# Kernel optimization log

Measured on AMD Instinct MI355X. Metric: run time of the kernel, lower is better.

The kernel has to match this reference:

```python
import jax, jax.numpy as jnp
import numpy as np

N = 100000      # nodes
E = 1600000     # graph edges
P = 800000      # hypergraph incidence pairs
HE = 20000      # hyperedges
F_IN = 128      # node features
DIM = 64        # hidden dim (hard-coded in module)
NC = 40         # num_classes


def _lin_init(key, fan_in, fan_out):
    k1, k2 = jax.random.split(key)
    s = 1.0 / np.sqrt(fan_in)
    W = jax.random.uniform(k1, (fan_in, fan_out), jnp.float32, -s, s)
    b = jax.random.uniform(k2, (fan_out,), jnp.float32, -s, s)
    return W, b


def setup_inputs() -> dict:
    key = jax.random.key(0)
    ks = jax.random.split(key, 10)
    x = jax.random.normal(ks[0], (N, F_IN), jnp.float32)
    edge_index = jax.random.randint(ks[1], (2, E), 0, N, dtype=jnp.int64)
    node_idx = jax.random.randint(ks[2], (P,), 0, N, dtype=jnp.int64)
    he_idx = jax.random.randint(ks[3], (P,), 0, HE, dtype=jnp.int64)
    hyperedge_index = jnp.stack([node_idx, he_idx], axis=0)
    W_h1, b_h1 = _lin_init(ks[4], F_IN, DIM)
    W_h2, b_h2 = _lin_init(ks[5], DIM, DIM)
    W_c1, b_c1 = _lin_init(ks[6], F_IN + DIM, DIM)
    W_c2, b_c2 = _lin_init(ks[7], DIM, NC)
    W_lp, b_lp = _lin_init(ks[8], NC, NC)
    return dict(x=x, edge_index=edge_index, hyperedge_index=hyperedge_index,
                W_h1=W_h1, b_h1=b_h1, W_h2=W_h2, b_h2=b_h2,
                W_c1=W_c1, b_c1=b_c1, W_c2=W_c2, b_c2=b_c2,
                W_lp=W_lp, b_lp=b_lp)


def hypergraph_conv(x, node_idx, he_idx, W, b):
    # PyG HypergraphConv (no attention, hyperedge_weight = 1):
    # out = D^{-1} H B^{-1} H^T (x W) + b
    xw = x @ W                                    # [N, D]
    ones = jnp.ones(node_idx.shape[0], xw.dtype)
    Dn = jax.ops.segment_sum(ones, node_idx, num_segments=N)   # node degree
    Bh = jax.ops.segment_sum(ones, he_idx, num_segments=HE)    # hyperedge size
    D_inv = jnp.where(Dn > 0, 1.0 / Dn, 0.0)
    B_inv = jnp.where(Bh > 0, 1.0 / Bh, 0.0)
    # node -> hyperedge: m_e = (1/|e|) sum_{i in e} xw[i]
    msg1 = xw[node_idx] * B_inv[he_idx][:, None]               # [P, D]
    e_feat = jax.ops.segment_sum(msg1, he_idx, num_segments=HE)
    # hyperedge -> node: out_i = (1/deg(i)) sum_{e ni i} m_e
    msg2 = e_feat[he_idx] * D_inv[node_idx][:, None]           # [P, D]
    out = jax.ops.segment_sum(msg2, node_idx, num_segments=N)
    return out + b


def gcn_conv(x, edge_index, W, b):
    # PyG GCNConv: add self-loops, symmetric normalization
    xw = x @ W                                    # [N, D]
    loop = jnp.arange(N, dtype=edge_index.dtype)
    src = jnp.concatenate([edge_index[0], loop])
    dst = jnp.concatenate([edge_index[1], loop])
    deg = jax.ops.segment_sum(jnp.ones(dst.shape[0], xw.dtype), dst, num_segments=N)
    dis = jnp.where(deg > 0, jax.lax.rsqrt(deg), 0.0)
    norm = dis[src] * dis[dst]                    # [E+N]
    out = jax.ops.segment_sum(xw[src] * norm[:, None], dst, num_segments=N)
    return out + b


def reference(x, edge_index, hyperedge_index,
              W_h1, b_h1, W_h2, b_h2, W_c1, b_c1, W_c2, b_c2, W_lp, b_lp):
    node_idx, he_idx = hyperedge_index[0], hyperedge_index[1]
    x_hyper = jax.nn.relu(hypergraph_conv(x, node_idx, he_idx, W_h1, b_h1))
    # dropout is identity in eval mode
    x_hyper = hypergraph_conv(x_hyper, node_idx, he_idx, W_h2, b_h2)
    xc = jnp.concatenate([x, x_hyper], axis=1)    # [N, F_IN + DIM]
    x_gnn = jax.nn.relu(gcn_conv(xc, edge_index, W_c1, b_c1))
    x_gnn = gcn_conv(x_gnn, edge_index, W_c2, b_c2)
    return x_gnn @ W_lp + b_lp                     # [N, NC]
```

## Files before the change

### kernel.cpp

```cpp
#include <hip/hip_runtime.h>
#include <hip/hip_bf16.h>


typedef __attribute__((ext_vector_type(8))) short s16x8;
typedef __attribute__((ext_vector_type(4))) float f32x4;
typedef __attribute__((ext_vector_type(8))) float f32x8;

__device__ __forceinline__ float ldf(const void* p, int f32, long long i) {
    if (f32) return ((const float*)p)[i];
    unsigned v = ((unsigned)((const unsigned short*)p)[i]) << 16;
    return __uint_as_float(v);
}

__device__ __forceinline__ int ldi(const int* __restrict__ w, int i64, long long i, int lim) {
    int v = i64 ? w[2 * i] : w[i];
    return ((unsigned)v < (unsigned)lim) ? v : 0;
}

__device__ __forceinline__ float b2f(unsigned short u) {
    return __uint_as_float(((unsigned)u) << 16);
}
__device__ __forceinline__ unsigned short f2b(float f) {
    __hip_bfloat16 h = __float2bfloat16(f);
    return *reinterpret_cast<unsigned short*>(&h);
}
__device__ __forceinline__ f32x8 b2f8(s16x8 u) {
    f32x8 r;
#pragma unroll
    for (int q = 0; q < 8; q++) r[q] = b2f((unsigned short)u[q]);
    return r;
}
__device__ __forceinline__ s16x8 f2b8(f32x8 v) {
    s16x8 r;
#pragma unroll
    for (int q = 0; q < 8; q++) r[q] = (short)f2b(v[q]);
    return r;
}

struct DPtrs { const void* p[13]; int n[13]; };

__global__ void detect_k(DPtrs dp, int* __restrict__ flags) {
    int b = blockIdx.x;
    __shared__ int cnt;
    if (threadIdx.x == 0) cnt = 0;
    __syncthreads();
    int c = 0;
    if (b < 11) {
        const unsigned short* u = (const unsigned short*)dp.p[b];
        int np = dp.n[b]; if (np > 2048) np = 2048;
        for (int i = threadIdx.x; i < np; i += blockDim.x) {
            unsigned e = (u[i] >> 7) & 0xFFu;
            if (e != 0u && (e < 90u || e > 160u)) c++;
        }
        atomicAdd(&cnt, c);
        __syncthreads();
        if (threadIdx.x == 0) flags[b] = (cnt * 8 > np) ? 1 : 0;
    } else {
        const int* w = (const int*)dp.p[b];
        int np = dp.n[b]; if (np > 1024) np = 1024;
        for (int i = threadIdx.x; i < np; i += blockDim.x)
            if (w[2 * i + 1] != 0) c++;
        atomicAdd(&cnt, c);
        __syncthreads();
        if (threadIdx.x == 0) flags[b] = (cnt == 0) ? 1 : 0;
    }
}

struct Item { int b1; unsigned p1; int b2; unsigned p2; };

__device__ __forceinline__ Item decode(const int* __restrict__ ew, const int* __restrict__ hw,
                                       const int* __restrict__ FL, long long i,
                                       int E, int P, int N, int HE, int shN, int shH) {
    Item it; it.b2 = -1; it.p2 = 0;
    if (i < E) {
        int g = FL[11];
        int key = ldi(ew, g, (long long)E + i, N);
        int val = ldi(ew, g, i, N);
        it.b1 = key >> shN;
        it.p1 = ((unsigned)(key & ((1 << shN) - 1)) << 20) | (unsigned)val;
    } else {
        long long j = i - E;
        int g = FL[12];
        int nd = ldi(hw, g, j, N);
        int he = ldi(hw, g, (long long)P + j, HE);
        it.b1 = 256 + (nd >> shN);
        it.p1 = ((unsigned)(nd & ((1 << shN) - 1)) << 20) | (unsigned)he;
        it.b2 = 512 + (he >> shH);
        it.p2 = ((unsigned)(he & ((1 << shH) - 1)) << 20) | (unsigned)nd;
    }
    return it;
}

#define PCHUNK 8192
#define PTHREADS 1024

__global__ __launch_bounds__(PTHREADS)
void chunkhist_k(const int* __restrict__ ew, const int* __restrict__ hw,
                 const int* __restrict__ FL, int* __restrict__ gcnt,
                 int* __restrict__ chunkHist,
                 int E, int P, int N, int HE, int shN, int shH) {
    __shared__ int hist[768];
    int t = threadIdx.x;
    for (int b = t; b < 768; b += PTHREADS) hist[b] = 0;
    __syncthreads();
    long long T = (long long)E + P;
    long long start = (long long)blockIdx.x * PCHUNK;
    long long end = start + PCHUNK; if (end > T) end = T;
    for (long long i = start + t; i < end; i += PTHREADS) {
        Item it = decode(ew, hw, FL, i, E, P, N, HE, shN, shH);
        atomicAdd(&hist[it.b1], 1);
        if (it.b2 >= 0) atomicAdd(&hist[it.b2], 1);
    }
    __syncthreads();
    long long hbase = (long long)blockIdx.x * 768;
    for (int b = t; b < 768; b += PTHREADS) {
        int h = hist[b];
        chunkHist[hbase + b] = h;
        if (h) atomicAdd(&gcnt[b], h);
    }
}

__global__ void bucket_scan_k(const int* __restrict__ gcnt, int* __restrict__ bkOff,
                              int* __restrict__ gcur, int E, int P) {
    __shared__ int sh[256];
    int t = threadIdx.x;
    long long rbase[3] = {0, (long long)E, (long long)E + P};
    for (int c = 0; c < 3; c++) {
        int v = gcnt[c * 256 + t];
        sh[t] = v;
        __syncthreads();
        for (int o = 1; o < 256; o <<= 1) {
            int y = (t >= o) ? sh[t - o] : 0;
            __syncthreads();
            sh[t] += y;
            __syncthreads();
        }
        int excl = sh[t] - v;
        bkOff[c * 256 + t] = excl;
        gcur[c * 256 + t] = (int)(rbase[c] + excl);
        __syncthreads();
    }
}

__global__ __launch_bounds__(PTHREADS)
void place_k(const int* __restrict__ ew, const int* __restrict__ hw,
             const int* __restrict__ FL, int* __restrict__ gcur,
             const int* __restrict__ chunkHist, unsigned* __restrict__ pbuf,
             int E, int P, int N, int HE, int shN, int shH) {
    __shared__ int cur[768];
    long long T = (long long)E + P;
    long long start = (long long)blockIdx.x * PCHUNK;
    long long end = start + PCHUNK; if (end > T) end = T;
    int t = threadIdx.x;
    long long hbase = (long long)blockIdx.x * 768;
    for (int b = t; b < 768; b += PTHREADS) {
        int h = chunkHist[hbase + b];
        cur[b] = h ? atomicAdd(&gcur[b], h) : 0;
    }
    __syncthreads();
    for (long long i = start + t; i < end; i += PTHREADS) {
        Item it = decode(ew, hw, FL, i, E, P, N, HE, shN, shH);
        int s1 = atomicAdd(&cur[it.b1], 1);
        pbuf[s1] = it.p1;
        if (it.b2 >= 0) {
            int s2 = atomicAdd(&cur[it.b2], 1);
            pbuf[s2] = it.p2;
        }
    }
}

__global__ void build_k(const unsigned* __restrict__ pbuf,
                        const int* __restrict__ gcnt, const int* __restrict__ bkOff,
                        int* __restrict__ eoff, int* __restrict__ ecnt, int* __restrict__ esrc,
                        int* __restrict__ poffN, int* __restrict__ pcntN, int* __restrict__ pheL,
                        int* __restrict__ poffH, int* __restrict__ pcntH, int* __restrict__ pniL,
                        float* __restrict__ dis, float* __restrict__ Dinv, float* __restrict__ Binv,
                        int E, int P, int N, int HE, int shN, int shH) {
    __shared__ int hist[512];
    __shared__ int offs[512];
    __shared__ int s2[256];
    int b = blockIdx.x, t = threadIdx.x;
    int csr = b >> 8, lb = b & 255;
    int sh    = (csr == 2) ? shH : shN;
    int nkeys = (csr == 2) ? HE : N;
    int span = 1 << sh;
    int keyBase = lb << sh;
    if (keyBase >= nkeys) return;
    int keyEnd = keyBase + span; if (keyEnd > nkeys) keyEnd = nkeys;
    int cnt = gcnt[b];
    long long rbase = (csr == 0) ? 0 : ((csr == 1) ? (long long)E : (long long)E + P);
    long long pstart = rbase + bkOff[b];
    int lstBase = bkOff[b];
    int* off  = (csr == 0) ? eoff : ((csr == 1) ? poffN : poffH);
    int* cntA = (csr == 0) ? ecnt : ((csr == 1) ? pcntN : pcntH);
    int* lst  = (csr == 0) ? esrc : ((csr == 1) ? pheL : pniL);

    for (int k = t; k < 512; k += 256) hist[k] = 0;
    __syncthreads();
    for (int i = t; i < cnt; i += 256)
        atomicAdd(&hist[pbuf[pstart + i] >> 20], 1);
    __syncthreads();
    int a0 = hist[2 * t], a1 = hist[2 * t + 1];
    s2[t] = a0 + a1;
    __syncthreads();
    for (int o = 1; o < 256; o <<= 1) {
        int y = (t >= o) ? s2[t - o] : 0;
        __syncthreads();
        s2[t] += y;
        __syncthreads();
    }
    int excl = s2[t] - (a0 + a1);
    offs[2 * t] = excl;
    offs[2 * t + 1] = excl + a0;
    __syncthreads();
    for (int k = keyBase + t; k < keyEnd; k += 256) {
        int h = hist[k - keyBase];
        off[k]  = lstBase + offs[k - keyBase];
        cntA[k] = h;
        if (csr == 0)      dis[k]  = rsqrtf((float)(h + 1));
        else if (csr == 1) Dinv[k] = h ? (1.f / (float)h) : 0.f;
        else               Binv[k] = h ? (1.f / (float)h) : 0.f;
    }
    __syncthreads();
    for (int i = t; i < cnt; i += 256) {
        unsigned u = pbuf[pstart + i];
        int lk = u >> 20;
        int slot = atomicAdd(&offs[lk], 1);
        lst[lstBase + slot] = (int)(u & 0xFFFFFu);
    }
}

struct BP { const void* B; const int* fB; int K; int M; int Mp; unsigned short* out; };

__global__ void prep_k(BP p0, BP p1, BP p2,
                       const void* Wc2, const int* fWc2, const void* Wlp, const int* fWlp,
                       const void* bc2, const int* fbc2, const void* blp, const int* fblp,
                       unsigned short* __restrict__ btl, float* __restrict__ bias2, int NC) {
    int t = threadIdx.x;
    if (blockIdx.x < 3) {
        BP p = (blockIdx.x == 0) ? p0 : (blockIdx.x == 1) ? p1 : p2;
        int fb = p.fB ? p.fB[0] : 1;
        int tot = p.Mp * p.K;
        for (int e = t; e < tot; e += blockDim.x) {
            int m = e / p.K, k = e - m * p.K;
            float v = (m < p.M) ? ldf(p.B, fb, (long long)k * p.M + m) : 0.f;
            p.out[e] = f2b(v);
        }
        return;
    }
    extern __shared__ float sm[];
    float* sW2 = sm;
    float* sLP = sm + 64 * NC;
    int fw2 = fWc2[0], flp = fWlp[0];
    for (int e = t; e < 64 * NC; e += blockDim.x) sW2[e] = ldf(Wc2, fw2, e);
    for (int e = t; e < NC * NC; e += blockDim.x) sLP[e] = ldf(Wlp, flp, e);
    for (int e = t; e < 48 * 64; e += blockDim.x) btl[e] = 0;
    __syncthreads();
    for (int e = t; e < 64 * NC; e += blockDim.x) {
        int r = e / NC, c = e % NC;
        float s = 0.f;
        for (int k = 0; k < NC; k++) s = fmaf(sW2[r * NC + k], sLP[k * NC + c], s);
        btl[c * 64 + r] = f2b(s);
    }
    if (t < NC) {
        float s = ldf(blp, fblp[0], t);
        int fb2 = fbc2[0];
        for (int k = 0; k < NC; k++) s = fmaf(ldf(bc2, fb2, k), sLP[k * NC + t], s);
        bias2[t] = s;
    }
}

__global__ void gat_n2e_k(const unsigned short* __restrict__ xw, const int* __restrict__ off,
                          const int* __restrict__ cnt, const int* __restrict__ lst,
                          const float* __restrict__ Binv, unsigned short* __restrict__ ef, int HE) {
    int idx = blockIdx.x * blockDim.x + threadIdx.x;
    int e = idx >> 3, l = idx & 7;
    if (e >= HE) return;
    int o = off[e], c = cnt[e];
    f32x8 a = {0.f, 0.f, 0.f, 0.f, 0.f, 0.f, 0.f, 0.f};
    int j = 0;
    for (; j + 4 <= c; j += 4) {
        int s0 = lst[o + j], s1 = lst[o + j + 1], s2 = lst[o + j + 2], s3 = lst[o + j + 3];
        f32x8 v0 = b2f8(*(const s16x8*)&xw[((long long)s0 << 6) + l * 8]);
        f32x8 v1 = b2f8(*(const s16x8*)&xw[((long long)s1 << 6) + l * 8]);
        f32x8 v2 = b2f8(*(const s16x8*)&xw[((long long)s2 << 6) + l * 8]);
        f32x8 v3 = b2f8(*(const s16x8*)&xw[((long long)s3 << 6) + l * 8]);
#pragma unroll
        for (int q = 0; q < 8; q++) a[q] += (v0[q] + v1[q]) + (v2[q] + v3[q]);
    }
    for (; j < c; j++) {
        f32x8 v = b2f8(*(const s16x8*)&xw[((long long)lst[o + j] << 6) + l * 8]);
#pragma unroll
        for (int q = 0; q < 8; q++) a[q] += v[q];
    }
    float bi = Binv[e];
#pragma unroll
    for (int q = 0; q < 8; q++) a[q] *= bi;
    *(s16x8*)&ef[((long long)e << 6) + l * 8] = f2b8(a);
}

template <bool RELU>
__global__ void gat_e2n_k(const unsigned short* __restrict__ ef, const int* __restrict__ off,
                          const int* __restrict__ cnt, const int* __restrict__ lst,
                          const float* __restrict__ Dinv, const void* __restrict__ bias,
                          const int* __restrict__ fb, unsigned short* __restrict__ out, int N) {
    int idx = blockIdx.x * blockDim.x + threadIdx.x;
    int w = idx >> 3, l = idx & 7;
    if (w >= N) return;
    int o = off[w], c = cnt[w];
    f32x8 a = {0.f, 0.f, 0.f, 0.f, 0.f, 0.f, 0.f, 0.f};
    int j = 0;
    for (; j + 4 <= c; j += 4) {
        int s0 = lst[o + j], s1 = lst[o + j + 1], s2 = lst[o + j + 2], s3 = lst[o + j + 3];
        f32x8 v0 = b2f8(*(const s16x8*)&ef[((long long)s0 << 6) + l * 8]);
        f32x8 v1 = b2f8(*(const s16x8*)&ef[((long long)s1 << 6) + l * 8]);
        f32x8 v2 = b2f8(*(const s16x8*)&ef[((long long)s2 << 6) + l * 8]);
        f32x8 v3 = b2f8(*(const s16x8*)&ef[((long long)s3 << 6) + l * 8]);
#pragma unroll
        for (int q = 0; q < 8; q++) a[q] += (v0[q] + v1[q]) + (v2[q] + v3[q]);
    }
    for (; j < c; j++) {
        f32x8 v = b2f8(*(const s16x8*)&ef[((long long)lst[o + j] << 6) + l * 8]);
#pragma unroll
        for (int q = 0; q < 8; q++) a[q] += v[q];
    }
    float di = Dinv[w];
    int fbv = fb[0];
#pragma unroll
    for (int q = 0; q < 8; q++) {
        float bq = ldf(bias, fbv, l * 8 + q);
        a[q] = a[q] * di + bq;
        if (RELU) a[q] = fmaxf(a[q], 0.f);
    }
    *(s16x8*)&out[((long long)w << 6) + l * 8] = f2b8(a);
}

template <bool RELU>
__global__ void gcn_gat_k(const unsigned short* __restrict__ y, const int* __restrict__ off,
                          const int* __restrict__ cnt, const int* __restrict__ lst,
                          const float* __restrict__ dis, const void* __restrict__ bias,
                          const int* __restrict__ fb, unsigned short* __restrict__ out, int N) {
    int idx = blockIdx.x * blockDim.x + threadIdx.x;
    int w = idx >> 3, l = idx & 7;
    if (w >= N) return;
    int o = off[w], c = cnt[w];
    f32x8 a = b2f8(*(const s16x8*)&y[((long long)w << 6) + l * 8]);
    int j = 0;
    for (; j + 4 <= c; j += 4) {
        int s0 = lst[o + j], s1 = lst[o + j + 1], s2 = lst[o + j + 2], s3 = lst[o + j + 3];
        f32x8 v0 = b2f8(*(const s16x8*)&y[((long long)s0 << 6) + l * 8]);
        f32x8 v1 = b2f8(*(const s16x8*)&y[((long long)s1 << 6) + l * 8]);
        f32x8 v2 = b2f8(*(const s16x8*)&y[((long long)s2 << 6) + l * 8]);
        f32x8 v3 = b2f8(*(const s16x8*)&y[((long long)s3 << 6) + l * 8]);
#pragma unroll
        for (int q = 0; q < 8; q++) a[q] += (v0[q] + v1[q]) + (v2[q] + v3[q]);
    }
    for (; j < c; j++) {
        f32x8 v = b2f8(*(const s16x8*)&y[((long long)lst[o + j] << 6) + l * 8]);
#pragma unroll
        for (int q = 0; q < 8; q++) a[q] += v[q];
    }
    float dd = dis[w];
    int fbv = fb[0];
#pragma unroll
    for (int q = 0; q < 8; q++) {
        float bq = ldf(bias, fbv, l * 8 + q);
        a[q] = a[q] * dd + bq;
        if (RELU) a[q] = fmaxf(a[q], 0.f);
    }
    *(s16x8*)&out[((long long)w << 6) + l * 8] = f2b8(a);
}

__global__ void gcn_gatM_k(const unsigned short* __restrict__ y2, const int* __restrict__ off,
                           const int* __restrict__ cnt, const int* __restrict__ lst,
                           const float* __restrict__ dis, const float* __restrict__ bias2,
                           float4* __restrict__ out4, int N, int NC) {
    int idx = blockIdx.x * blockDim.x + threadIdx.x;
    int wave = idx >> 6, l64 = idx & 63;
    int lpr = NC >> 3;
    int rpw = 64 / lpr;
    int grp = l64 / lpr, li = l64 - grp * lpr;
    int w = wave * rpw + grp;
    if (grp >= rpw || w >= N) return;
    int o = off[w], c = cnt[w];
    f32x8 a = b2f8(*(const s16x8*)&y2[(long long)w * NC + li * 8]);
    int j = 0;
    for (; j + 4 <= c; j += 4) {
        int s0 = lst[o + j], s1 = lst[o + j + 1], s2 = lst[o + j + 2], s3 = lst[o + j + 3];
        f32x8 v0 = b2f8(*(const s16x8*)&y2[(long long)s0 * NC + li * 8]);
        f32x8 v1 = b2f8(*(const s16x8*)&y2[(long long)s1 * NC + li * 8]);
        f32x8 v2 = b2f8(*(const s16x8*)&y2[(long long)s2 * NC + li * 8]);
        f32x8 v3 = b2f8(*(const s16x8*)&y2[(long long)s3 * NC + li * 8]);
#pragma unroll
        for (int q = 0; q < 8; q++) a[q] += (v0[q] + v1[q]) + (v2[q] + v3[q]);
    }
    for (; j < c; j++) {
        f32x8 v = b2f8(*(const s16x8*)&y2[(long long)lst[o + j] * NC + li * 8]);
#pragma unroll
        for (int q = 0; q < 8; q++) a[q] += v[q];
    }
    float dd = dis[w];
    const float4* b4 = (const float4*)&bias2[li * 8];
    float4 b0 = b4[0], b1 = b4[1];
    float4 lo = make_float4(a[0] * dd + b0.x, a[1] * dd + b0.y, a[2] * dd + b0.z, a[3] * dd + b0.w);
    float4 hi = make_float4(a[4] * dd + b1.x, a[5] * dd + b1.y, a[6] * dd + b1.z, a[7] * dd + b1.w);
    long long base = ((long long)w * NC + li * 8) >> 2;
    out4[base] = lo;
    out4[base + 1] = hi;
}

__device__ __forceinline__ s16x8 load8bf(const void* A, int af, long long base) {
    s16x8 o;
    if (af) {
        float4 v0 = *(const float4*)((const float*)A + base);
        float4 v1 = *(const float4*)((const float*)A + base + 4);
        o[0] = (short)f2b(v0.x); o[1] = (short)f2b(v0.y);
        o[2] = (short)f2b(v0.z); o[3] = (short)f2b(v0.w);
        o[4] = (short)f2b(v1.x); o[5] = (short)f2b(v1.y);
        o[6] = (short)f2b(v1.z); o[7] = (short)f2b(v1.w);
    } else {
        o = *(const s16x8*)&((const unsigned short*)A)[base];
    }
    return o;
}

template <int KK, int MM, bool CATMODE, bool ABF16, bool SCALE>
__global__ __launch_bounds__(256)
void gemm_mfma2_k(const void* __restrict__ A, const int* __restrict__ fA,
                  const unsigned short* __restrict__ A2,
                  const unsigned short* __restrict__ Bt,
                  const float* __restrict__ dscale,
                  unsigned short* __restrict__ C, int NR) {
    constexpr int MT = (MM + 15) / 16;
    static_assert(KK % 32 == 0, "K must be multiple of 32");

    const int t = threadIdx.x;
    const int wid = t >> 6, lane = t & 63;
    const long long r0 = ((long long)blockIdx.x * 4 + wid) * 32;
    if (r0 >= NR) return;

    const int af = fA ? fA[0] : 1;
    const int arow = lane & 15;
    const int kgrp = lane >> 4;
    long long ra = r0 + arow;      if (ra > NR - 1) ra = NR - 1;
    long long rb = r0 + 16 + arow; if (rb > NR - 1) rb = NR - 1;

    f32x4 acc0[MT] = {};
    f32x4 acc1[MT] = {};
#pragma unroll
    for (int kc = 0; kc < KK; kc += 32) {
        const int kb = kc + kgrp * 8;
        s16x8 a0, a1;
        if constexpr (CATMODE) {
            if (kc < 128) {
                a0 = load8bf(A, af, ra * 128 + kb);
                a1 = load8bf(A, af, rb * 128 + kb);
            } else {
                a0 = *(const s16x8*)&A2[ra * 64 + (kb - 128)];
                a1 = *(const s16x8*)&A2[rb * 64 + (kb - 128)];
            }
        } else if constexpr (ABF16) {
            a0 = *(const s16x8*)&((const unsigned short*)A)[ra * KK + kb];
            a1 = *(const s16x8*)&((const unsigned short*)A)[rb * KK + kb];
        } else {
            a0 = load8bf(A, af, ra * (long long)KK + kb);
            a1 = load8bf(A, af, rb * (long long)KK + kb);
        }
#pragma unroll
        for (int m = 0; m < MT; m++) {
            s16x8 b = *(const s16x8*)&Bt[(m * 16 + arow) * KK + kb];
            acc0[m] = __builtin_amdgcn_mfma_f32_16x16x32_bf16(a0, b, acc0[m], 0, 0, 0);
            acc1[m] = __builtin_amdgcn_mfma_f32_16x16x32_bf16(a1, b, acc1[m], 0, 0, 0);
        }
    }

    const int col0 = lane & 15;
    const int rsub = (lane >> 4) * 4;
#pragma unroll
    for (int h = 0; h < 2; h++) {
#pragma unroll
        for (int i = 0; i < 4; i++) {
            long long r = r0 + h * 16 + rsub + i;
            if (r < NR) {
                float s = SCALE ? dscale[r] : 1.f;
#pragma unroll
                for (int m = 0; m < MT; m++) {
                    int col = m * 16 + col0;
                    float val = h ? acc1[m][i] : acc0[m][i];
                    if (MT * 16 == MM || col < MM)
                        C[r * MM + col] = f2b(val * s);
                }
            }
        }
    }
}

static inline dim3 g1d(long long n, int b) { return dim3((unsigned)((n + b - 1) / b)); }
static inline int imin(int a, int b) { return a < b ? a : b; }

extern "C" void kernel_launch(void* const* d_in, const int* in_sizes, int n_in,
                              void* d_out, int out_size, void* d_ws, size_t ws_size,
                              hipStream_t stream) {
    const int N  = in_sizes[0] / 128;
    const int E  = in_sizes[1] / 2;
    const int P  = in_sizes[2] / 2;
    const int HE = 20000;
    const int NC = in_sizes[9] / 64;

    const void* x    = d_in[0];
    const int*  ew   = (const int*)d_in[1];
    const int*  hw   = (const int*)d_in[2];
    const void* W_h1 = d_in[3];
    const void* b_h1 = d_in[4];
    const void* W_h2 = d_in[5];
    const void* b_h2 = d_in[6];
    const void* W_c1 = d_in[7];
    const void* b_c1 = d_in[8];
    const void* W_c2 = d_in[9];
    const void* b_c2 = d_in[10];
    const void* W_lp = d_in[11];
    const void* b_lp = d_in[12];

    int shN = 0; while (((N - 1) >> shN) >= 256) shN++;
    int shH = 0; while (((HE - 1) >> shH) >= 256) shH++;

    long long T = (long long)E + P;
    int nChunks = (int)((T + PCHUNK - 1) / PCHUNK);

    char* wp = (char*)d_ws;
    auto allocF = [&](size_t n) { float* p = (float*)wp; wp += n * 4; return p; };
    auto allocI = [&](size_t n) { int* p = (int*)wp; wp += n * 4; return p; };
    unsigned short* ub  = (unsigned short*)allocF((size_t)N * 32);
    unsigned short* hb  = (unsigned short*)allocF((size_t)N * 32);
    unsigned short* efb = (unsigned short*)allocF((size_t)HE * 32);
    float* dis   = allocF(N);
    float* Dinv  = allocF(N);
    float* Binv  = allocF(HE);
    float* bias2 = allocF(NC);
    unsigned short* bt1 = (unsigned short*)allocF((size_t)64 * 128 / 2);
    unsigned short* bt2 = (unsigned short*)allocF((size_t)64 * 64 / 2);
    unsigned short* btc = (unsigned short*)allocF((size_t)64 * 192 / 2);
    unsigned short* btl = (unsigned short*)allocF((size_t)48 * 64 / 2);
    int* ecnt  = allocI(N);
    int* pcntN = allocI(N);
    int* pcntH = allocI(HE);
    int* eoff  = allocI(N);
    int* poffN = allocI(N);
    int* poffH = allocI(HE);
    int* esrc  = allocI(E);
    int* pheL  = allocI(P);
    int* pniL  = allocI(P);
    int* gBkt  = allocI(768);
    int* bkOff = allocI(768);
    int* gcur  = allocI(768);
    int* FL    = allocI(16);
    int* chunkHist = allocI((size_t)nChunks * 768);
    unsigned* pbuf = (unsigned*)allocI((size_t)E + 2 * (size_t)P);

    dim3 b256(256), b1024(PTHREADS), d1(1);

    DPtrs dp;
    const void* farr[11] = {x, W_h1, b_h1, W_h2, b_h2, W_c1, b_c1, W_c2, b_c2, W_lp, b_lp};
    const int   fsz[11]  = {in_sizes[0], in_sizes[3], in_sizes[4], in_sizes[5], in_sizes[6],
                            in_sizes[7], in_sizes[8], in_sizes[9], in_sizes[10], in_sizes[11],
                            in_sizes[12]};
    for (int i = 0; i < 11; ++i) { dp.p[i] = farr[i]; dp.n[i] = fsz[i]; }
    dp.p[11] = ew; dp.n[11] = imin(E, 1024);
    dp.p[12] = hw; dp.n[12] = imin(P, 1024);
    detect_k<<<dim3(13), b256, 0, stream>>>(dp, FL);
    const int* fX   = FL + 0;
    const int* fWh1 = FL + 1,  *fbh1 = FL + 2;
    const int* fWh2 = FL + 3,  *fbh2 = FL + 4;
    const int* fWc1 = FL + 5,  *fbc1 = FL + 6;
    const int* fWc2 = FL + 7,  *fbc2 = FL + 8;
    const int* fWlp = FL + 9,  *fblp = FL + 10;

    {
        BP p0 = {W_h1, fWh1, 128, 64, 64, bt1};
        BP p1 = {W_h2, fWh2,  64, 64, 64, bt2};
        BP p2 = {W_c1, fWc1, 192, 64, 64, btc};
        prep_k<<<dim3(4), b256, (64 * NC + NC * NC) * 4, stream>>>(
            p0, p1, p2, W_c2, fWc2, W_lp, fWlp, b_c2, fbc2, b_lp, fblp, btl, bias2, NC);
    }

    hipMemsetAsync(gBkt, 0, 768 * 4, stream);
    chunkhist_k<<<dim3(nChunks), b1024, 0, stream>>>(ew, hw, FL, gBkt, chunkHist,
                                                     E, P, N, HE, shN, shH);
    bucket_scan_k<<<d1, b256, 0, stream>>>(gBkt, bkOff, gcur, E, P);
    place_k<<<dim3(nChunks), b1024, 0, stream>>>(ew, hw, FL, gcur, chunkHist, pbuf,
                                                 E, P, N, HE, shN, shH);
    build_k<<<dim3(768), b256, 0, stream>>>(pbuf, gBkt, bkOff,
                                            eoff, ecnt, esrc,
                                            poffN, pcntN, pheL,
                                            poffH, pcntH, pniL,
                                            dis, Dinv, Binv,
                                            E, P, N, HE, shN, shH);

    const dim3 mfmaGrid((N + 127) / 128);
    const dim3 gatN8(g1d((long long)N * 8, 256));
    const dim3 gatH8(g1d((long long)HE * 8, 256));
    const int rpw = 64 / (NC >> 3);
    const dim3 gatNC(g1d((long long)((N + rpw - 1) / rpw) * 64, 256));

    gemm_mfma2_k<128, 64, false, false, false><<<mfmaGrid, b256, 0, stream>>>(
        x, fX, nullptr, bt1, nullptr, ub, N);
    gat_n2e_k<<<gatH8, b256, 0, stream>>>(ub, poffH, pcntH, pniL, Binv, efb, HE);
    gat_e2n_k<true><<<gatN8, b256, 0, stream>>>(efb, poffN, pcntN, pheL, Dinv, b_h1, fbh1, hb, N);

    gemm_mfma2_k<64, 64, false, true, false><<<mfmaGrid, b256, 0, stream>>>(
        hb, nullptr, nullptr, bt2, nullptr, ub, N);
    gat_n2e_k<<<gatH8, b256, 0, stream>>>(ub, poffH, pcntH, pniL, Binv, efb, HE);
    gat_e2n_k<false><<<gatN8, b256, 0, stream>>>(efb, poffN, pcntN, pheL, Dinv, b_h2, fbh2, hb, N);

    gemm_mfma2_k<192, 64, true, false, true><<<mfmaGrid, b256, 0, stream>>>(
        x, fX, hb, btc, dis, ub, N);
    gcn_gat_k<true><<<gatN8, b256, 0, stream>>>(ub, eoff, ecnt, esrc, dis, b_c1, fbc1, hb, N);

    gemm_mfma2_k<64, 40, false, true, true><<<mfmaGrid, b256, 0, stream>>>(
        hb, nullptr, nullptr, btl, dis, ub, N);
    gcn_gatM_k<<<gatNC, b256, 0, stream>>>(ub, eoff, ecnt, esrc, dis, bias2, (float4*)d_out, N, NC);
}
```

Measured before the change: 409.0 us.

## Fuse bucket scan into histogram via last-block pattern and batch gather indices with shuffles

The bucket counter reset moves into detect_k, which removes a memset, and the one-block bucket scan is folded into the tail of chunkhist_k using a last-block-done counter. Together these drop a launch and a memset from the stream. The gather kernels now load eight neighbor indices with one coalesced per-lane load, broadcast them with wave shuffles, and issue eight row loads before accumulating, which raises memory-level parallelism. The 40-class GCN gather does the same in groups of five. The risks are extra register pressure from eight in-flight vectors and relying on a threadfence and atomic read for cross-block visibility in the scan.

```diff
diff --git a/kernel.cpp b/kernel.cpp
--- a/kernel.cpp
+++ b/kernel.cpp
@@ -39,8 +39,13 @@
 
 struct DPtrs { const void* p[13]; int n[13]; };
 
-__global__ void detect_k(DPtrs dp, int* __restrict__ flags) {
+__global__ void detect_k(DPtrs dp, int* __restrict__ flags,
+                         int* __restrict__ gBkt, int* __restrict__ done) {
     int b = blockIdx.x;
+    if (b == 0) {
+        for (int i = threadIdx.x; i < 768; i += blockDim.x) gBkt[i] = 0;
+        if (threadIdx.x == 0) done[0] = 0;
+    }
     __shared__ int cnt;
     if (threadIdx.x == 0) cnt = 0;
     __syncthreads();
@@ -97,7 +102,8 @@
 __global__ __launch_bounds__(PTHREADS)
 void chunkhist_k(const int* __restrict__ ew, const int* __restrict__ hw,
                  const int* __restrict__ FL, int* __restrict__ gcnt,
-                 int* __restrict__ chunkHist,
+                 int* __restrict__ chunkHist, int* __restrict__ done,
+                 int* __restrict__ bkOff, int* __restrict__ gcur,
                  int E, int P, int N, int HE, int shN, int shH) {
     __shared__ int hist[768];
     int t = threadIdx.x;
@@ -118,26 +124,31 @@
         chunkHist[hbase + b] = h;
         if (h) atomicAdd(&gcnt[b], h);
     }
-}
-
-__global__ void bucket_scan_k(const int* __restrict__ gcnt, int* __restrict__ bkOff,
-                              int* __restrict__ gcur, int E, int P) {
+    __syncthreads();
+    __shared__ int isLast;
+    if (t == 0) {
+        __threadfence();
+        isLast = (atomicAdd(done, 1) == (int)gridDim.x - 1);
+    }
+    __syncthreads();
+    if (!isLast) return;
     __shared__ int sh[256];
-    int t = threadIdx.x;
-    long long rbase[3] = {0, (long long)E, (long long)E + P};
     for (int c = 0; c < 3; c++) {
-        int v = gcnt[c * 256 + t];
-        sh[t] = v;
+        int v = 0;
+        if (t < 256) { v = atomicAdd(&gcnt[c * 256 + t], 0); sh[t] = v; }
         __syncthreads();
         for (int o = 1; o < 256; o <<= 1) {
-            int y = (t >= o) ? sh[t - o] : 0;
+            int y = (t < 256 && t >= o) ? sh[t - o] : 0;
             __syncthreads();
-            sh[t] += y;
+            if (t < 256) sh[t] += y;
             __syncthreads();
         }
-        int excl = sh[t] - v;
-        bkOff[c * 256 + t] = excl;
-        gcur[c * 256 + t] = (int)(rbase[c] + excl);
+        if (t < 256) {
+            int excl = sh[t] - v;
+            bkOff[c * 256 + t] = excl;
+            long long rb = (c == 0) ? 0 : ((c == 1) ? (long long)E : (long long)E + P);
+            gcur[c * 256 + t] = (int)(rb + excl);
+        }
         __syncthreads();
     }
 }
@@ -270,29 +281,43 @@
     }
 }
 
+__device__ __forceinline__ f32x8 gather_sum(const unsigned short* __restrict__ src,
+                                            const int* __restrict__ lst,
+                                            int o, int c, int l, int lbase, f32x8 a) {
+    int j = 0;
+    for (; j + 8 <= c; j += 8) {
+        int myi = lst[o + j + l];
+        int si[8];
+#pragma unroll
+        for (int q = 0; q < 8; q++) si[q] = __shfl(myi, lbase + q, 64);
+        s16x8 d[8];
+#pragma unroll
+        for (int q = 0; q < 8; q++)
+            d[q] = *(const s16x8*)&src[((long long)si[q] << 6) + l * 8];
+#pragma unroll
+        for (int q = 0; q < 8; q++) {
+            f32x8 v = b2f8(d[q]);
+#pragma unroll
+            for (int r = 0; r < 8; r++) a[r] += v[r];
+        }
+    }
+    for (; j < c; j++) {
+        f32x8 v = b2f8(*(const s16x8*)&src[((long long)lst[o + j] << 6) + l * 8]);
+#pragma unroll
+        for (int r = 0; r < 8; r++) a[r] += v[r];
+    }
+    return a;
+}
+
 __global__ void gat_n2e_k(const unsigned short* __restrict__ xw, const int* __restrict__ off,
                           const int* __restrict__ cnt, const int* __restrict__ lst,
                           const float* __restrict__ Binv, unsigned short* __restrict__ ef, int HE) {
     int idx = blockIdx.x * blockDim.x + threadIdx.x;
     int e = idx >> 3, l = idx & 7;
     if (e >= HE) return;
-    int o = off[e], c = cnt[e];
+    int lbase = (threadIdx.x & 63) & ~7;
     f32x8 a = {0.f, 0.f, 0.f, 0.f, 0.f, 0.f, 0.f, 0.f};
-    int j = 0;
-    for (; j + 4 <= c; j += 4) {
-        int s0 = lst[o + j], s1 = lst[o + j + 1], s2 = lst[o + j + 2], s3 = lst[o + j + 3];
-        f32x8 v0 = b2f8(*(const s16x8*)&xw[((long long)s0 << 6) + l * 8]);
-        f32x8 v1 = b2f8(*(const s16x8*)&xw[((long long)s1 << 6) + l * 8]);
-        f32x8 v2 = b2f8(*(const s16x8*)&xw[((long long)s2 << 6) + l * 8]);
-        f32x8 v3 = b2f8(*(const s16x8*)&xw[((long long)s3 << 6) + l * 8]);
-#pragma unroll
-        for (int q = 0; q < 8; q++) a[q] += (v0[q] + v1[q]) + (v2[q] + v3[q]);
-    }
-    for (; j < c; j++) {
-        f32x8 v = b2f8(*(const s16x8*)&xw[((long long)lst[o + j] << 6) + l * 8]);
-#pragma unroll
-        for (int q = 0; q < 8; q++) a[q] += v[q];
-    }
+    a = gather_sum(xw, lst, off[e], cnt[e], l, lbase, a);
     float bi = Binv[e];
 #pragma unroll
     for (int q = 0; q < 8; q++) a[q] *= bi;
@@ -307,23 +332,9 @@
     int idx = blockIdx.x * blockDim.x + threadIdx.x;
     int w = idx >> 3, l = idx & 7;
     if (w >= N) return;
-    int o = off[w], c = cnt[w];
+    int lbase = (threadIdx.x & 63) & ~7;
     f32x8 a = {0.f, 0.f, 0.f, 0.f, 0.f, 0.f, 0.f, 0.f};
-    int j = 0;
-    for (; j + 4 <= c; j += 4) {
-        int s0 = lst[o + j], s1 = lst[o + j + 1], s2 = lst[o + j + 2], s3 = lst[o + j + 3];
-        f32x8 v0 = b2f8(*(const s16x8*)&ef[((long long)s0 << 6) + l * 8]);
-        f32x8 v1 = b2f8(*(const s16x8*)&ef[((long long)s1 << 6) + l * 8]);
-        f32x8 v2 = b2f8(*(const s16x8*)&ef[((long long)s2 << 6) + l * 8]);
-        f32x8 v3 = b2f8(*(const s16x8*)&ef[((long long)s3 << 6) + l * 8]);
-#pragma unroll
-        for (int q = 0; q < 8; q++) a[q] += (v0[q] + v1[q]) + (v2[q] + v3[q]);
-    }
-    for (; j < c; j++) {
-        f32x8 v = b2f8(*(const s16x8*)&ef[((long long)lst[o + j] << 6) + l * 8]);
-#pragma unroll
-        for (int q = 0; q < 8; q++) a[q] += v[q];
-    }
+    a = gather_sum(ef, lst, off[w], cnt[w], l, lbase, a);
     float di = Dinv[w];
     int fbv = fb[0];
 #pragma unroll
@@ -343,23 +354,9 @@
     int idx = blockIdx.x * blockDim.x + threadIdx.x;
     int w = idx >> 3, l = idx & 7;
     if (w >= N) return;
-    int o = off[w], c = cnt[w];
+    int lbase = (threadIdx.x & 63) & ~7;
     f32x8 a = b2f8(*(const s16x8*)&y[((long long)w << 6) + l * 8]);
-    int j = 0;
-    for (; j + 4 <= c; j += 4) {
-        int s0 = lst[o + j], s1 = lst[o + j + 1], s2 = lst[o + j + 2], s3 = lst[o + j + 3];
-        f32x8 v0 = b2f8(*(const s16x8*)&y[((long long)s0 << 6) + l * 8]);
-        f32x8 v1 = b2f8(*(const s16x8*)&y[((long long)s1 << 6) + l * 8]);
-        f32x8 v2 = b2f8(*(const s16x8*)&y[((long long)s2 << 6) + l * 8]);
-        f32x8 v3 = b2f8(*(const s16x8*)&y[((long long)s3 << 6) + l * 8]);
-#pragma unroll
-        for (int q = 0; q < 8; q++) a[q] += (v0[q] + v1[q]) + (v2[q] + v3[q]);
-    }
-    for (; j < c; j++) {
-        f32x8 v = b2f8(*(const s16x8*)&y[((long long)lst[o + j] << 6) + l * 8]);
-#pragma unroll
-        for (int q = 0; q < 8; q++) a[q] += v[q];
-    }
+    a = gather_sum(y, lst, off[w], cnt[w], l, lbase, a);
     float dd = dis[w];
     int fbv = fb[0];
 #pragma unroll
@@ -383,21 +380,29 @@
     int w = wave * rpw + grp;
     if (grp >= rpw || w >= N) return;
     int o = off[w], c = cnt[w];
+    int lbase = l64 - li;
     f32x8 a = b2f8(*(const s16x8*)&y2[(long long)w * NC + li * 8]);
     int j = 0;
-    for (; j + 4 <= c; j += 4) {
-        int s0 = lst[o + j], s1 = lst[o + j + 1], s2 = lst[o + j + 2], s3 = lst[o + j + 3];
-        f32x8 v0 = b2f8(*(const s16x8*)&y2[(long long)s0 * NC + li * 8]);
-        f32x8 v1 = b2f8(*(const s16x8*)&y2[(long long)s1 * NC + li * 8]);
-        f32x8 v2 = b2f8(*(const s16x8*)&y2[(long long)s2 * NC + li * 8]);
-        f32x8 v3 = b2f8(*(const s16x8*)&y2[(long long)s3 * NC + li * 8]);
-#pragma unroll
-        for (int q = 0; q < 8; q++) a[q] += (v0[q] + v1[q]) + (v2[q] + v3[q]);
+    for (; j + 5 <= c; j += 5) {
+        int myi = lst[o + j + li];
+        int si[5];
+#pragma unroll
+        for (int q = 0; q < 5; q++) si[q] = __shfl(myi, lbase + q, 64);
+        s16x8 d[5];
+#pragma unroll
+        for (int q = 0; q < 5; q++)
+            d[q] = *(const s16x8*)&y2[(long long)si[q] * NC + li * 8];
+#pragma unroll
+        for (int q = 0; q < 5; q++) {
+            f32x8 v = b2f8(d[q]);
+#pragma unroll
+            for (int r = 0; r < 8; r++) a[r] += v[r];
+        }
     }
     for (; j < c; j++) {
         f32x8 v = b2f8(*(const s16x8*)&y2[(long long)lst[o + j] * NC + li * 8]);
 #pragma unroll
-        for (int q = 0; q < 8; q++) a[q] += v[q];
+        for (int r = 0; r < 8; r++) a[r] += v[r];
     }
     float dd = dis[w];
     const float4* b4 = (const float4*)&bias2[li * 8];
@@ -554,6 +559,7 @@
     int* bkOff = allocI(768);
     int* gcur  = allocI(768);
     int* FL    = allocI(16);
+    int* done  = allocI(4);
     int* chunkHist = allocI((size_t)nChunks * 768);
     unsigned* pbuf = (unsigned*)allocI((size_t)E + 2 * (size_t)P);
 
@@ -567,7 +573,7 @@
     for (int i = 0; i < 11; ++i) { dp.p[i] = farr[i]; dp.n[i] = fsz[i]; }
     dp.p[11] = ew; dp.n[11] = imin(E, 1024);
     dp.p[12] = hw; dp.n[12] = imin(P, 1024);
-    detect_k<<<dim3(13), b256, 0, stream>>>(dp, FL);
+    detect_k<<<dim3(13), b256, 0, stream>>>(dp, FL, gBkt, done);
     const int* fX   = FL + 0;
     const int* fWh1 = FL + 1,  *fbh1 = FL + 2;
     const int* fWh2 = FL + 3,  *fbh2 = FL + 4;
@@ -583,10 +589,8 @@
             p0, p1, p2, W_c2, fWc2, W_lp, fWlp, b_c2, fbc2, b_lp, fblp, btl, bias2, NC);
     }
 
-    hipMemsetAsync(gBkt, 0, 768 * 4, stream);
-    chunkhist_k<<<dim3(nChunks), b1024, 0, stream>>>(ew, hw, FL, gBkt, chunkHist,
-                                                     E, P, N, HE, shN, shH);
-    bucket_scan_k<<<d1, b256, 0, stream>>>(gBkt, bkOff, gcur, E, P);
+    chunkhist_k<<<dim3(nChunks), b1024, 0, stream>>>(ew, hw, FL, gBkt, chunkHist, done,
+                                                     bkOff, gcur, E, P, N, HE, shN, shH);
     place_k<<<dim3(nChunks), b1024, 0, stream>>>(ew, hw, FL, gcur, chunkHist, pbuf,
                                                  E, P, N, HE, shN, shH);
     build_k<<<dim3(768), b256, 0, stream>>>(pbuf, gBkt, bkOff,
```

Result: slower. 425.7 us (+4.1%).
